# Optimization experiments

Hardware: AMD Instinct MI355X
Metric: run time of the kernel (lower is better)

The kernel has to match this reference:

```python
import jax, jax.numpy as jnp
import numpy as np

# ---- configuration matching init_kwargs ----
CTX_C = 96        # context_v_features
M_FREQS = 8       # m_encode_num_freqs
OUT_C = 45        # out_features
NDIM = 3
SIGMA = 5.0       # sigma_encode_scale
EPS = 1e-7        # TARGET_COORD_EPSILON
CX = CY = CZ = 32
QX = QY = QZ = 48
B = 1
CTX_VOX = 2.0
Q_VOX = 1.25
N_COORD = 4 * NDIM + NDIM * 2 * M_FREQS   # 60
INTERNAL = CTX_C + N_COORD                # 156


def _lin_init(k, fi, fo):
    s = 1.0 / np.sqrt(fi)
    kw, kb = jax.random.split(k)
    return (jax.random.uniform(kw, (fi, fo), jnp.float32, -s, s),
            jax.random.uniform(kb, (fo,), jnp.float32, -s, s))


def setup_inputs() -> dict:
    key = jax.random.key(0)
    ks = jax.random.split(key, 12)
    context_v = jax.random.normal(ks[0], (B, CTX_C, CX, CY, CZ), jnp.float32)
    ax = jnp.arange(CX, dtype=jnp.float32) * CTX_VOX
    gx, gy, gz = jnp.meshgrid(ax, ax, ax, indexing='ij')
    context_spatial_extent = jnp.broadcast_to(
        jnp.stack([gx, gy, gz], 0)[None], (B, 3, CX, CY, CZ)).astype(jnp.float32)
    # queries in the interior so nearest-idx + 1 stays in bounds
    query_coord = jax.random.uniform(ks[1], (B, 3, QX, QY, QZ), jnp.float32,
                                     CTX_VOX, (CX - 2) * CTX_VOX)
    query_vox_size = jnp.full((B, 3), Q_VOX, jnp.float32)
    inp = dict(context_v=context_v, context_spatial_extent=context_spatial_extent,
               query_vox_size=query_vox_size, query_coord=query_coord)
    ki = 2
    for b in range(2):
        inp[f'blk{b}_w0'], inp[f'blk{b}_b0'] = _lin_init(ks[ki], INTERNAL, CTX_C); ki += 1
        inp[f'blk{b}_w1'], inp[f'blk{b}_b1'] = _lin_init(ks[ki], CTX_C, CTX_C); ki += 1
        inp[f'blk{b}_w2'], inp[f'blk{b}_b2'] = _lin_init(ks[ki], CTX_C, CTX_C); ki += 1
    inp['post_w'], inp['post_b'] = _lin_init(ks[ki], CTX_C, OUT_C)
    return inp


def _flat(t):
    # 'b c x y z -> (b x y z) c'
    return jnp.moveaxis(t, 1, -1).reshape(-1, t.shape[1])


def _unflat(t, b, x, y, z):
    # '(b x y z) c -> b c x y z'
    return jnp.moveaxis(t.reshape(b, x, y, z, -1), -1, 1)


def _fourier(c):
    # c: (N, 3) normalized coords; geometric frequency ladder scaled by sigma
    freqs = SIGMA ** (jnp.arange(M_FREQS, dtype=c.dtype) / M_FREQS)   # (m,)
    ang = (2.0 * jnp.pi) * c[:, :, None] * freqs                      # (N,3,m)
    return jnp.concatenate([jnp.sin(ang), jnp.cos(ang)], axis=-1).reshape(c.shape[0], -1)


def _skip_block(x, coord, w0, b0, w1, b1, w2, b2):
    # SkipMLPBlock: concat(context, coord) -> 3 dense SiLU layers -> residual add
    h = jnp.concatenate([x, coord], axis=-1)
    h = jax.nn.silu(h @ w0 + b0)
    h = jax.nn.silu(h @ w1 + b1)
    h = jax.nn.silu(h @ w2 + b2)
    return x + h, coord


def _sub_grid_forward(ctx_val, ctx_coord, q_coord, ctx_vox, q_vox, p):
    # ctx_val: (B,C,X,Y,Z); coords: (B,3,X,Y,Z); ctx_vox/q_vox: (B,3,1,1,1)
    b, _, x, y, z = q_coord.shape
    rel = jnp.maximum(ctx_coord - q_coord, -ctx_vox / 2 + EPS)
    rel_norm = (rel - jnp.min(rel, axis=(2, 3, 4), keepdims=True)) / (1.5 * ctx_vox)
    enc = _fourier(_flat(rel_norm))                                   # (N, 6m)
    qv = jnp.broadcast_to(q_vox, rel_norm.shape)
    coord_feats = jnp.concatenate(
        [_flat(qv), _flat(ctx_coord), _flat(q_coord), _flat(rel_norm), enc], axis=-1)
    h = _flat(ctx_val)
    xc = coord_feats
    for i in range(2):
        h, xc = _skip_block(h, xc, p[f'blk{i}_w0'], p[f'blk{i}_b0'],
                            p[f'blk{i}_w1'], p[f'blk{i}_b1'],
                            p[f'blk{i}_w2'], p[f'blk{i}_b2'])
    pred = h @ p['post_w'] + p['post_b']
    return _unflat(pred, b, x, y, z), rel


def reference(context_v, context_spatial_extent, query_vox_size, query_coord,
              blk0_w0, blk0_b0, blk0_w1, blk0_b1, blk0_w2, blk0_b2,
              blk1_w0, blk1_b0, blk1_w1, blk1_b1, blk1_w2, blk1_b2,
              post_w, post_b):
    p = dict(blk0_w0=blk0_w0, blk0_b0=blk0_b0, blk0_w1=blk0_w1, blk0_b1=blk0_b1,
             blk0_w2=blk0_w2, blk0_b2=blk0_b2, blk1_w0=blk1_w0, blk1_b0=blk1_b0,
             blk1_w1=blk1_w1, blk1_b1=blk1_b1, blk1_w2=blk1_w2, blk1_b2=blk1_b2,
             post_w=post_w, post_b=post_b)
    bsz, _, qx, qy, qz = query_coord.shape
    cx, cy, cz = context_spatial_extent.shape[2:]
    ctx_vox = jnp.abs(context_spatial_extent[..., 1, 1, 1]
                      - context_spatial_extent[..., 0, 0, 0])[:, :, None, None, None]
    q_vox = query_vox_size[:, :, None, None, None]
    # nearest context voxel index per query point (regular grid)
    origin = context_spatial_extent[:, :, 0, 0, 0][:, :, None, None, None]
    nearest = jnp.round((query_coord - origin) / ctx_vox).astype(jnp.int32)
    xi = jnp.clip(nearest[:, 0], 0, cx - 2).reshape(-1)
    yi = jnp.clip(nearest[:, 1], 0, cy - 2).reshape(-1)
    zi = jnp.clip(nearest[:, 2], 0, cz - 2).reshape(-1)
    b_idx = jnp.broadcast_to(jnp.arange(bsz)[:, None, None, None],
                             (bsz, qx, qy, qz)).reshape(-1)
    preds = []
    rel000 = None
    for i in (0, 1):
        for j in (0, 1):
            for k in (0, 1):
                cval = context_v[b_idx, :, xi + i, yi + j, zi + k]            # (N,C) gather
                cval = _unflat(cval, bsz, qx, qy, qz)
                ccoord = context_spatial_extent[b_idx, :, xi + i, yi + j, zi + k]
                ccoord = _unflat(ccoord, bsz, qx, qy, qz)
                pred, rel = _sub_grid_forward(cval, ccoord, query_coord,
                                              ctx_vox, q_vox, p)
                preds.append(pred)
                if i == 0 and j == 0 and k == 0:
                    rel000 = rel
    preds = jnp.stack(preds, 0)   # (8, B, OUT, X, Y, Z)
    # trilinear combine over the 2x2x2 sub-window (grid_sample align_corners=True;
    # grid coord channel 0 indexes z_sub (W), 1 -> y_sub (H), 2 -> x_sub (D))
    g = jnp.clip((rel000 - 0.5) * 2.0, -1.0 + EPS, 1.0 - EPS)
    t = (g + 1.0) / 2.0
    tz, ty, tx = t[:, 0], t[:, 1], t[:, 2]
    out = jnp.zeros_like(preds[0])
    for i in (0, 1):
        wi = tx if i == 1 else 1.0 - tx
        for j in (0, 1):
            wj = ty if j == 1 else 1.0 - ty
            for k in (0, 1):
                wk = tz if k == 1 else 1.0 - tz
                out = out + preds[i * 4 + j * 2 + k] * (wi * wj * wk)[:, None]
    return out
```

## Files before the change

### kernel.cpp

```cpp
#include <hip/hip_runtime.h>
#include <hip/hip_bf16.h>

typedef unsigned short ushort_t;
typedef short short8 __attribute__((ext_vector_type(8)));
typedef short shrt4 __attribute__((ext_vector_type(4)));
typedef unsigned short ush4 __attribute__((ext_vector_type(4)));
typedef unsigned int uintx2 __attribute__((ext_vector_type(2)));
typedef float floatx4 __attribute__((ext_vector_type(4)));

#define SA 168
#define SW 104
#define NQ 110592
#define CVOL 32768

#define L0A   0
#define L0B   15360
#define A1_00 30720
#define A1_01 39936
#define A1_10 49152
#define A1_11 58368
#define PST   67584
#define WTOT  72192
#define BTOT  9216

#define WSW_OFF  64
#define BIAS_OFF 147456
#define CVT_OFF  196608

#if defined(__HIP_DEVICE_COMPILE__)
#define MFMA16(A, B, C) __builtin_amdgcn_mfma_f32_16x16x16bf16_1k(A, B, C, 0, 0, 0)
#else
#define MFMA16(A, B, C) (C)
#endif

#if defined(__HIP_DEVICE_COMPILE__) && __has_builtin(__builtin_amdgcn_sinf) && __has_builtin(__builtin_amdgcn_cosf) && __has_builtin(__builtin_amdgcn_fractf)
#define FAST_SINCOS 1
#else
#define FAST_SINCOS 0
#endif

__device__ __forceinline__ float bf2f(ushort_t u) { return __uint_as_float(((unsigned)u) << 16); }
__device__ __forceinline__ ushort_t f2bf(float f) {
    unsigned u = __float_as_uint(f);
    unsigned r = (u + 0x7fffu + ((u >> 16) & 1u)) >> 16;
    return (ushort_t)r;
}
__device__ __forceinline__ shrt4 pk4(floatx4 v) {
    uintx2 u;
    u[0] = (unsigned)f2bf(v[0]) | ((unsigned)f2bf(v[1]) << 16);
    u[1] = (unsigned)f2bf(v[2]) | ((unsigned)f2bf(v[3]) << 16);
    return __builtin_bit_cast(shrt4, u);
}
__device__ __forceinline__ unsigned encodeMin(float x) {
    unsigned u = __float_as_uint(x);
    return (u & 0x80000000u) ? ~u : (u | 0x80000000u);
}
__device__ __forceinline__ float decodeMin(unsigned key) {
    unsigned u = (key & 0x80000000u) ? (key ^ 0x80000000u) : ~key;
    return __uint_as_float(u);
}

__device__ __constant__ float FREQ[8] = {
    1.0f, 1.2228445f, 1.4953488f, 1.8285791f,
    2.2360680f, 2.7343640f, 3.3437015f, 4.0888269f
};

__global__ void decoder_txp(const float* __restrict__ cv, ushort_t* __restrict__ cvT) {
    __shared__ ushort_t ld[128 * SW];
    int tid = threadIdx.x;
    int base = blockIdx.x * 128;
    int cl = tid & 127, h = tid >> 7;
    #pragma unroll 4
    for (int ch = h * 48; ch < h * 48 + 48; ++ch)
        ld[cl * SW + ch] = f2bf(cv[ch * CVOL + base + cl]);
    __syncthreads();
    #pragma unroll
    for (int it = 0; it < 6; ++it) {
        int idx = it * 256 + tid;
        int r = idx / 12, c = idx - r * 12;
        *(uint4*)&cvT[(base + r) * 96 + c * 8] = *(const uint4*)&ld[r * SW + c * 8];
    }
}

__global__ void decoder_prep(const float* __restrict__ w00, const float* __restrict__ b00,
                             const float* __restrict__ w01, const float* __restrict__ b01,
                             const float* __restrict__ w02, const float* __restrict__ b02,
                             const float* __restrict__ w10, const float* __restrict__ b10,
                             const float* __restrict__ w11, const float* __restrict__ b11,
                             const float* __restrict__ w12, const float* __restrict__ b12,
                             const float* __restrict__ pw, ushort_t* __restrict__ wsW,
                             float* __restrict__ biasF, unsigned* __restrict__ keys) {
    int idx = blockIdx.x * 256 + threadIdx.x;
    if (idx < 3) keys[idx] = 0xFFFFFFFFu;
    if (idx >= WTOT + BTOT) return;
    if (idx >= WTOT) {
        int t = idx - WTOT;
        int layer = t / 1536, rem = t - layer * 1536;
        int mt = rem >> 8, l2i = rem & 255;
        int lane = l2i >> 2, r = l2i & 3;
        int m = mt * 16 + (lane >> 4) * 4 + r;
        const float* B = layer == 0 ? b00 : layer == 1 ? b01 : layer == 2 ? b02
                       : layer == 3 ? b10 : layer == 4 ? b11 : b12;
        biasF[t] = B[m];
        return;
    }
    ushort_t v = 0;
    if (idx < A1_00) {
        const float* W = (idx < L0B) ? w00 : w10;
        int li = idx - ((idx < L0B) ? L0A : L0B);
        int j = li & 7, lane = (li >> 3) & 63, chunk = li >> 9;
        int kc = chunk % 5, mt = chunk / 5;
        int k = kc * 32 + (lane >> 4) * 8 + j;
        int m = mt * 16 + (lane & 15);
        if (k < 156) v = f2bf(W[k * 96 + m]);
    } else if (idx < PST) {
        const float* W = idx < A1_01 ? w01 : idx < A1_10 ? w02 : idx < A1_11 ? w11 : w12;
        int off = idx < A1_01 ? A1_00 : idx < A1_10 ? A1_01 : idx < A1_11 ? A1_10 : A1_11;
        int li = idx - off;
        int i = li & 3, kl = (li >> 2) & 1, lane = (li >> 3) & 63, chunk = li >> 9;
        int kp = chunk % 3, mt = chunk / 3;
        int k = (kp * 2 + kl) * 16 + (lane >> 4) * 4 + i;
        int m = mt * 16 + (lane & 15);
        v = f2bf(W[k * 96 + m]);
    } else {
        int li = idx - PST;
        int j = li & 7, lane = (li >> 3) & 63, chunk = li >> 9;
        int kc = chunk % 3, t = chunk / 3;
        int k = kc * 32 + (lane >> 4) * 8 + j;
        int n = t * 16 + (lane & 15);
        if (n < 45) v = f2bf(pw[k * 45 + n]);
    }
    wsW[idx] = v;
}

__global__ void decoder_prepass(const float* __restrict__ qc, const float* __restrict__ ext,
                                unsigned* __restrict__ keys) {
    __shared__ unsigned mk[3];
    int tid = threadIdx.x;
    int lane = tid & 63;
    if (tid < 3) mk[tid] = 0xFFFFFFFFu;
    __syncthreads();
    int p = blockIdx.x * 256 + tid;
    #pragma unroll
    for (int c = 0; c < 3; ++c) {
        float org = ext[c * CVOL];
        float vox = fabsf(ext[c * CVOL + 1057] - org);
        float q = qc[c * NQ + p];
        float nf = rintf((q - org) / vox);
        int ci = (int)nf; ci = ci < 0 ? 0 : (ci > 30 ? 30 : ci);
        float base = org + (float)ci * vox - q;
        for (int off = 32; off > 0; off >>= 1) base = fminf(base, __shfl_xor(base, off));
        if (lane == 0) atomicMin(&mk[c], encodeMin(base));
    }
    __syncthreads();
    if (tid < 3) atomicMin(&keys[tid], mk[tid]);
}

__global__ __launch_bounds__(256, 3) void decoder_main(
    const ushort_t* __restrict__ cvT, const float* __restrict__ ext,
    const float* __restrict__ qvx, const float* __restrict__ qc,
    const float* __restrict__ pb, const ushort_t* __restrict__ wsW,
    const float* __restrict__ biasF,
    const unsigned* __restrict__ minKeys, float* __restrict__ out)
{
    __shared__ ushort_t Xin[128 * SA];
    __shared__ ushort_t Hhat[16 * SW];
    __shared__ float ptQ[3][16], ptBase[3][16], ptT[3][16];
    __shared__ int ptCI[3][16];
    __shared__ float wcorn[16][8];

    const int tid = threadIdx.x;
    const int lane = tid & 63;
    const int wv = tid >> 6;
    const int quad = lane >> 4;
    const int l16 = lane & 15;
    const int lane8 = lane << 3, quad8 = quad * 8, quad4 = quad * 4;
    const int p0 = blockIdx.x * 16;
    const int col0 = wv * 32;

    float vox[3], org[3], lim[3], inv3v[3], qv[3], mrel[3][2];
    #pragma unroll
    for (int c = 0; c < 3; ++c) {
        org[c] = ext[c * CVOL];
        vox[c] = fabsf(ext[c * CVOL + 1057] - org[c]);
        lim[c] = -0.5f * vox[c] + 1e-7f;
        inv3v[c] = 1.0f / (1.5f * vox[c]);
        qv[c] = qvx[c];
        float mb = decodeMin(minKeys[c]);
        mrel[c][0] = fmaxf(mb, lim[c]);
        mrel[c][1] = fmaxf(mb + vox[c], lim[c]);
    }

    if (tid < 64) {
        int p = tid >> 2, c = tid & 3;
        if (c < 3) {
            float q = qc[c * NQ + p0 + p];
            float nf = rintf((q - org[c]) / vox[c]);
            int ci = (int)nf; ci = ci < 0 ? 0 : (ci > 30 ? 30 : ci);
            float base = org[c] + (float)ci * vox[c] - q;
            float rel0 = fmaxf(base, lim[c]);
            float g = fminf(fmaxf((rel0 - 0.5f) * 2.0f, -1.0f + 1e-7f), 1.0f - 1e-7f);
            ptQ[c][p] = q; ptCI[c][p] = ci; ptBase[c][p] = base; ptT[c][p] = (g + 1.0f) * 0.5f;
        }
    }
    __syncthreads();

    if (tid < 128) {
        int p = tid >> 3, corner = tid & 7;
        int i = corner >> 2, j = (corner >> 1) & 1, k = corner & 1;
        float wx = i ? ptT[2][p] : 1.0f - ptT[2][p];
        float wy = j ? ptT[1][p] : 1.0f - ptT[1][p];
        float wz = k ? ptT[0][p] : 1.0f - ptT[0][p];
        wcorn[p][corner] = wx * wy * wz;
    }

    {
        const int r = tid >> 1, h = tid & 1;
        const int p = r >> 3, corner = r & 7;
        const int i0 = corner >> 2, i1 = (corner >> 1) & 1, i2 = corner & 1;
        int io[3] = {i0, i1, i2};

        int cell = (ptCI[0][p] + i0) * 1024 + (ptCI[1][p] + i1) * 32 + ptCI[2][p] + i2;
        const uint4* src = (const uint4*)&cvT[cell * 96];
        uint4* dstX = (uint4*)&Xin[r * SA];
        #pragma unroll
        for (int cc = h * 6; cc < h * 6 + 6; ++cc) dstX[cc] = src[cc];

        float rn[3];
        #pragma unroll
        for (int c = 0; c < 3; ++c) {
            float rel = fmaxf(ptBase[c][p] + (float)io[c] * vox[c], lim[c]);
            rn[c] = (rel - mrel[c][io[c]]) * inv3v[c];
        }
        ushort_t* row = &Xin[r * SA];
        if (h == 0) {
            #pragma unroll
            for (int c = 0; c < 3; ++c) {
                row[96 + c]  = f2bf(qv[c]);
                row[99 + c]  = f2bf(org[c] + (float)(ptCI[c][p] + io[c]) * vox[c]);
                row[102 + c] = f2bf(ptQ[c][p]);
                row[105 + c] = f2bf(rn[c]);
            }
            #pragma unroll
            for (int z = 156; z < SA; ++z) row[z] = 0;
            #pragma unroll
            for (int m = 0; m < 8; ++m) {
                float ang = rn[0] * FREQ[m];
#if FAST_SINCOS
                float fr = __builtin_amdgcn_fractf(ang);
                row[108 + m] = f2bf(__builtin_amdgcn_sinf(fr));
                row[116 + m] = f2bf(__builtin_amdgcn_cosf(fr));
#else
                float s, co; sincospif(2.0f * ang, &s, &co);
                row[108 + m] = f2bf(s); row[116 + m] = f2bf(co);
#endif
            }
        } else {
            #pragma unroll
            for (int c = 1; c < 3; ++c) {
                #pragma unroll
                for (int m = 0; m < 8; ++m) {
                    float ang = rn[c] * FREQ[m];
#if FAST_SINCOS
                    float fr = __builtin_amdgcn_fractf(ang);
                    row[108 + c * 16 + m] = f2bf(__builtin_amdgcn_sinf(fr));
                    row[108 + c * 16 + 8 + m] = f2bf(__builtin_amdgcn_cosf(fr));
#else
                    float s, co; sincospif(2.0f * ang, &s, &co);
                    row[108 + c * 16 + m] = f2bf(s);
                    row[108 + c * 16 + 8 + m] = f2bf(co);
#endif
                }
            }
        }
    }
    __syncthreads();

    const int A32off[2] = {L0A, L0B};
    const int A16off[2][2] = {{A1_00, A1_01}, {A1_10, A1_11}};
    floatx4 acc[6][2];
    shrt4 bfr[6][2];

    #pragma unroll
    for (int blk = 0; blk < 2; ++blk) {
        {
            short8 bX[2][5];
            #pragma unroll
            for (int nt = 0; nt < 2; ++nt)
                #pragma unroll
                for (int kc = 0; kc < 5; ++kc)
                    bX[nt][kc] = *(const short8*)&Xin[(col0 + nt * 16 + l16) * SA + kc * 32 + quad8];
            #pragma unroll
            for (int mt = 0; mt < 6; ++mt) {
                short8 aw[5];
                #pragma unroll
                for (int kc = 0; kc < 5; ++kc)
                    aw[kc] = *(const short8*)&wsW[A32off[blk] + ((mt * 5 + kc) << 9) + lane8];
                #pragma unroll
                for (int nt = 0; nt < 2; ++nt) {
                    floatx4 a = {0.f, 0.f, 0.f, 0.f};
                    #pragma unroll
                    for (int kc = 0; kc < 5; ++kc)
                        a = __builtin_amdgcn_mfma_f32_16x16x32_bf16(aw[kc], bX[nt][kc], a, 0, 0, 0);
                    acc[mt][nt] = a;
                }
            }
        }
        {
            const int lay = blk * 3;
            #pragma unroll
            for (int mt = 0; mt < 6; ++mt) {
                floatx4 bv = *(const floatx4*)&biasF[((lay * 6 + mt) << 8) + (lane << 2)];
                #pragma unroll
                for (int nt = 0; nt < 2; ++nt) {
                    floatx4 s;
                    #pragma unroll
                    for (int r = 0; r < 4; ++r) {
                        float z = acc[mt][nt][r] + bv[r];
                        s[r] = z * __builtin_amdgcn_rcpf(1.0f + __expf(-z));
                    }
                    bfr[mt][nt] = pk4(s);
                }
            }
        }
        #pragma unroll
        for (int l = 1; l < 3; ++l) {
            #pragma unroll
            for (int mt = 0; mt < 6; ++mt) {
                short8 awp[3];
                #pragma unroll
                for (int kp = 0; kp < 3; ++kp)
                    awp[kp] = *(const short8*)&wsW[A16off[blk][l - 1] + ((mt * 3 + kp) << 9) + lane8];
                #pragma unroll
                for (int nt = 0; nt < 2; ++nt) {
                    floatx4 a = {0.f, 0.f, 0.f, 0.f};
                    #pragma unroll
                    for (int kc = 0; kc < 6; ++kc) {
                        shrt4 af = (kc & 1)
                            ? __builtin_shufflevector(awp[kc >> 1], awp[kc >> 1], 4, 5, 6, 7)
                            : __builtin_shufflevector(awp[kc >> 1], awp[kc >> 1], 0, 1, 2, 3);
                        a = MFMA16(af, bfr[kc][nt], a);
                    }
                    acc[mt][nt] = a;
                }
            }
            const int lay = blk * 3 + l;
            if (l == 1) {
                #pragma unroll
                for (int mt = 0; mt < 6; ++mt) {
                    floatx4 bv = *(const floatx4*)&biasF[((lay * 6 + mt) << 8) + (lane << 2)];
                    #pragma unroll
                    for (int nt = 0; nt < 2; ++nt) {
                        floatx4 s;
                        #pragma unroll
                        for (int r = 0; r < 4; ++r) {
                            float z = acc[mt][nt][r] + bv[r];
                            s[r] = z * __builtin_amdgcn_rcpf(1.0f + __expf(-z));
                        }
                        bfr[mt][nt] = pk4(s);
                    }
                }
            } else {
                #pragma unroll
                for (int mt = 0; mt < 6; ++mt) {
                    floatx4 bv = *(const floatx4*)&biasF[((lay * 6 + mt) << 8) + (lane << 2)];
                    #pragma unroll
                    for (int nt = 0; nt < 2; ++nt) {
                        int ca = (col0 + nt * 16 + l16) * SA + mt * 16 + quad4;
                        ush4 hu = *(const ush4*)&Xin[ca];
                        floatx4 s;
                        #pragma unroll
                        for (int r = 0; r < 4; ++r) {
                            float z = acc[mt][nt][r] + bv[r];
                            s[r] = z * __builtin_amdgcn_rcpf(1.0f + __expf(-z)) + bf2f(hu[r]);
                        }
                        uintx2 w;
                        w[0] = (unsigned)f2bf(s[0]) | ((unsigned)f2bf(s[1]) << 16);
                        w[1] = (unsigned)f2bf(s[2]) | ((unsigned)f2bf(s[3]) << 16);
                        *(uintx2*)&Xin[ca] = w;
                    }
                }
            }
        }
    }

    {
        int p = tid >> 4, s6 = (tid & 15) * 6;
        float w8[8];
        #pragma unroll
        for (int c = 0; c < 8; ++c) w8[c] = wcorn[p][c];
        #pragma unroll
        for (int cc = 0; cc < 6; ++cc) {
            int col = s6 + cc;
            float sum = 0.f;
            #pragma unroll
            for (int c = 0; c < 8; ++c) sum += w8[c] * bf2f(Xin[(p * 8 + c) * SA + col]);
            Hhat[p * SW + col] = f2bf(sum);
        }
    }
    __syncthreads();

    if (wv < 3) {
        const ushort_t* wb = wsW + PST;
        floatx4 pacc = {0.f, 0.f, 0.f, 0.f};
        #pragma unroll
        for (int kc = 0; kc < 3; ++kc) {
            short8 a = *(const short8*)&Hhat[l16 * SW + kc * 32 + quad8];
            short8 bfrag = *(const short8*)&wb[((wv * 3 + kc) << 9) + lane8];
            pacc = __builtin_amdgcn_mfma_f32_16x16x32_bf16(a, bfrag, pacc, 0, 0, 0);
        }
        int n = 16 * wv + l16;
        if (n < 45) {
            float bv = pb[n];
            float4 v;
            v.x = pacc[0] + bv; v.y = pacc[1] + bv; v.z = pacc[2] + bv; v.w = pacc[3] + bv;
            *(float4*)&out[n * NQ + p0 + quad * 4] = v;
        }
    }
}

extern "C" void kernel_launch(void* const* d_in, const int* in_sizes, int n_in,
                              void* d_out, int out_size, void* d_ws, size_t ws_size,
                              hipStream_t stream) {
    (void)in_sizes; (void)n_in; (void)out_size; (void)ws_size;
    const float* cv  = (const float*)d_in[0];
    const float* ext = (const float*)d_in[1];
    const float* qvx = (const float*)d_in[2];
    const float* qc  = (const float*)d_in[3];
    const float* w00 = (const float*)d_in[4];
    const float* b00 = (const float*)d_in[5];
    const float* w01 = (const float*)d_in[6];
    const float* b01 = (const float*)d_in[7];
    const float* w02 = (const float*)d_in[8];
    const float* b02 = (const float*)d_in[9];
    const float* w10 = (const float*)d_in[10];
    const float* b10 = (const float*)d_in[11];
    const float* w11 = (const float*)d_in[12];
    const float* b11 = (const float*)d_in[13];
    const float* w12 = (const float*)d_in[14];
    const float* b12 = (const float*)d_in[15];
    const float* pw  = (const float*)d_in[16];
    const float* pb  = (const float*)d_in[17];

    unsigned* keys = (unsigned*)d_ws;
    ushort_t* wsW  = (ushort_t*)((char*)d_ws + WSW_OFF);
    float* biasF   = (float*)((char*)d_ws + BIAS_OFF);
    ushort_t* cvT  = (ushort_t*)((char*)d_ws + CVT_OFF);

    decoder_txp<<<256, 256, 0, stream>>>(cv, cvT);
    decoder_prep<<<318, 256, 0, stream>>>(w00, b00, w01, b01, w02, b02,
                                          w10, b10, w11, b11, w12, b12,
                                          pw, wsW, biasF, keys);
    decoder_prepass<<<432, 256, 0, stream>>>(qc, ext, keys);
    decoder_main<<<6912, 256, 0, stream>>>(cvT, ext, qvx, qc,
                                           pb, wsW, biasF, keys, (float*)d_out);
}
```

Before: 356.7 us.

## Merge prep kernels, fold bias into MFMA init, use packed bf16 conversions

Merges the three pre-processing kernels (transpose, weight prep, min-key prepass) into one launch that dispatches on block index, and initializes the keys with a memset instead. In the main kernel the bias is loaded as the MFMA accumulator's initial value instead of being added afterwards, float-to-bf16 packing uses a hardware packed-convert builtin when available, and the corner-weighted reduction reads bf16 pairs as 32-bit words. Together these aim to cut launch overhead and ALU work in the epilogues. The fallback pack rounds differently from round-to-nearest-even, and the memset adds a separate stream operation.

New measurement: 322.9 us. 1.1x faster.

```diff
diff --git a/kernel.cpp b/kernel.cpp
--- a/kernel.cpp
+++ b/kernel.cpp
@@ -27,6 +27,10 @@
 #define BIAS_OFF 147456
 #define CVT_OFF  196608
 
+#define TXP_NB   256
+#define PREP_NB  318
+#define PRE_NB   (TXP_NB + PREP_NB + 432)
+
 #if defined(__HIP_DEVICE_COMPILE__)
 #define MFMA16(A, B, C) __builtin_amdgcn_mfma_f32_16x16x16bf16_1k(A, B, C, 0, 0, 0)
 #else
@@ -45,10 +49,19 @@
     unsigned r = (u + 0x7fffu + ((u >> 16) & 1u)) >> 16;
     return (ushort_t)r;
 }
+__device__ __forceinline__ unsigned pkpair(float a, float b) {
+#if defined(__HIP_DEVICE_COMPILE__) && __has_builtin(__builtin_amdgcn_cvt_pk_bf16_f32)
+    return __builtin_bit_cast(unsigned, __builtin_amdgcn_cvt_pk_bf16_f32(a, b));
+#else
+    unsigned ua = __float_as_uint(a) + 0x8000u;
+    unsigned ub = __float_as_uint(b) + 0x8000u;
+    return __builtin_amdgcn_perm(ub, ua, 0x07060302);
+#endif
+}
 __device__ __forceinline__ shrt4 pk4(floatx4 v) {
     uintx2 u;
-    u[0] = (unsigned)f2bf(v[0]) | ((unsigned)f2bf(v[1]) << 16);
-    u[1] = (unsigned)f2bf(v[2]) | ((unsigned)f2bf(v[3]) << 16);
+    u[0] = pkpair(v[0], v[1]);
+    u[1] = pkpair(v[2], v[3]);
     return __builtin_bit_cast(shrt4, u);
 }
 __device__ __forceinline__ unsigned encodeMin(float x) {
@@ -65,95 +78,99 @@
     2.2360680f, 2.7343640f, 3.3437015f, 4.0888269f
 };
 
-__global__ void decoder_txp(const float* __restrict__ cv, ushort_t* __restrict__ cvT) {
+__global__ void decoder_pre(const float* __restrict__ cv, ushort_t* __restrict__ cvT,
+                            const float* __restrict__ w00, const float* __restrict__ b00,
+                            const float* __restrict__ w01, const float* __restrict__ b01,
+                            const float* __restrict__ w02, const float* __restrict__ b02,
+                            const float* __restrict__ w10, const float* __restrict__ b10,
+                            const float* __restrict__ w11, const float* __restrict__ b11,
+                            const float* __restrict__ w12, const float* __restrict__ b12,
+                            const float* __restrict__ pw, ushort_t* __restrict__ wsW,
+                            float* __restrict__ biasF,
+                            const float* __restrict__ qc, const float* __restrict__ ext,
+                            unsigned* __restrict__ keys) {
     __shared__ ushort_t ld[128 * SW];
-    int tid = threadIdx.x;
-    int base = blockIdx.x * 128;
-    int cl = tid & 127, h = tid >> 7;
-    #pragma unroll 4
-    for (int ch = h * 48; ch < h * 48 + 48; ++ch)
-        ld[cl * SW + ch] = f2bf(cv[ch * CVOL + base + cl]);
-    __syncthreads();
-    #pragma unroll
-    for (int it = 0; it < 6; ++it) {
-        int idx = it * 256 + tid;
-        int r = idx / 12, c = idx - r * 12;
-        *(uint4*)&cvT[(base + r) * 96 + c * 8] = *(const uint4*)&ld[r * SW + c * 8];
-    }
-}
-
-__global__ void decoder_prep(const float* __restrict__ w00, const float* __restrict__ b00,
-                             const float* __restrict__ w01, const float* __restrict__ b01,
-                             const float* __restrict__ w02, const float* __restrict__ b02,
-                             const float* __restrict__ w10, const float* __restrict__ b10,
-                             const float* __restrict__ w11, const float* __restrict__ b11,
-                             const float* __restrict__ w12, const float* __restrict__ b12,
-                             const float* __restrict__ pw, ushort_t* __restrict__ wsW,
-                             float* __restrict__ biasF, unsigned* __restrict__ keys) {
-    int idx = blockIdx.x * 256 + threadIdx.x;
-    if (idx < 3) keys[idx] = 0xFFFFFFFFu;
-    if (idx >= WTOT + BTOT) return;
-    if (idx >= WTOT) {
-        int t = idx - WTOT;
-        int layer = t / 1536, rem = t - layer * 1536;
-        int mt = rem >> 8, l2i = rem & 255;
-        int lane = l2i >> 2, r = l2i & 3;
-        int m = mt * 16 + (lane >> 4) * 4 + r;
-        const float* B = layer == 0 ? b00 : layer == 1 ? b01 : layer == 2 ? b02
-                       : layer == 3 ? b10 : layer == 4 ? b11 : b12;
-        biasF[t] = B[m];
+    __shared__ unsigned mk[3];
+    const int bx = blockIdx.x;
+    const int tid = threadIdx.x;
+
+    if (bx < TXP_NB) {
+        int base = bx * 128;
+        int cl = tid & 127, h = tid >> 7;
+        #pragma unroll 4
+        for (int ch = h * 48; ch < h * 48 + 48; ++ch)
+            ld[cl * SW + ch] = f2bf(cv[ch * CVOL + base + cl]);
+        __syncthreads();
+        #pragma unroll
+        for (int it = 0; it < 6; ++it) {
+            int idx = it * 256 + tid;
+            int r = idx / 12, c = idx - r * 12;
+            *(uint4*)&cvT[(base + r) * 96 + c * 8] = *(const uint4*)&ld[r * SW + c * 8];
+        }
         return;
     }
-    ushort_t v = 0;
-    if (idx < A1_00) {
-        const float* W = (idx < L0B) ? w00 : w10;
-        int li = idx - ((idx < L0B) ? L0A : L0B);
-        int j = li & 7, lane = (li >> 3) & 63, chunk = li >> 9;
-        int kc = chunk % 5, mt = chunk / 5;
-        int k = kc * 32 + (lane >> 4) * 8 + j;
-        int m = mt * 16 + (lane & 15);
-        if (k < 156) v = f2bf(W[k * 96 + m]);
-    } else if (idx < PST) {
-        const float* W = idx < A1_01 ? w01 : idx < A1_10 ? w02 : idx < A1_11 ? w11 : w12;
-        int off = idx < A1_01 ? A1_00 : idx < A1_10 ? A1_01 : idx < A1_11 ? A1_10 : A1_11;
-        int li = idx - off;
-        int i = li & 3, kl = (li >> 2) & 1, lane = (li >> 3) & 63, chunk = li >> 9;
-        int kp = chunk % 3, mt = chunk / 3;
-        int k = (kp * 2 + kl) * 16 + (lane >> 4) * 4 + i;
-        int m = mt * 16 + (lane & 15);
-        v = f2bf(W[k * 96 + m]);
-    } else {
-        int li = idx - PST;
-        int j = li & 7, lane = (li >> 3) & 63, chunk = li >> 9;
-        int kc = chunk % 3, t = chunk / 3;
-        int k = kc * 32 + (lane >> 4) * 8 + j;
-        int n = t * 16 + (lane & 15);
-        if (n < 45) v = f2bf(pw[k * 45 + n]);
-    }
-    wsW[idx] = v;
-}
-
-__global__ void decoder_prepass(const float* __restrict__ qc, const float* __restrict__ ext,
-                                unsigned* __restrict__ keys) {
-    __shared__ unsigned mk[3];
-    int tid = threadIdx.x;
-    int lane = tid & 63;
-    if (tid < 3) mk[tid] = 0xFFFFFFFFu;
-    __syncthreads();
-    int p = blockIdx.x * 256 + tid;
-    #pragma unroll
-    for (int c = 0; c < 3; ++c) {
-        float org = ext[c * CVOL];
-        float vox = fabsf(ext[c * CVOL + 1057] - org);
-        float q = qc[c * NQ + p];
-        float nf = rintf((q - org) / vox);
-        int ci = (int)nf; ci = ci < 0 ? 0 : (ci > 30 ? 30 : ci);
-        float base = org + (float)ci * vox - q;
-        for (int off = 32; off > 0; off >>= 1) base = fminf(base, __shfl_xor(base, off));
-        if (lane == 0) atomicMin(&mk[c], encodeMin(base));
-    }
-    __syncthreads();
-    if (tid < 3) atomicMin(&keys[tid], mk[tid]);
+    if (bx < TXP_NB + PREP_NB) {
+        int idx = (bx - TXP_NB) * 256 + tid;
+        if (idx >= WTOT + BTOT) return;
+        if (idx >= WTOT) {
+            int t = idx - WTOT;
+            int layer = t / 1536, rem = t - layer * 1536;
+            int mt = rem >> 8, l2i = rem & 255;
+            int lane = l2i >> 2, r = l2i & 3;
+            int m = mt * 16 + (lane >> 4) * 4 + r;
+            const float* B = layer == 0 ? b00 : layer == 1 ? b01 : layer == 2 ? b02
+                           : layer == 3 ? b10 : layer == 4 ? b11 : b12;
+            biasF[t] = B[m];
+            return;
+        }
+        ushort_t v = 0;
+        if (idx < A1_00) {
+            const float* W = (idx < L0B) ? w00 : w10;
+            int li = idx - ((idx < L0B) ? L0A : L0B);
+            int j = li & 7, lane = (li >> 3) & 63, chunk = li >> 9;
+            int kc = chunk % 5, mt = chunk / 5;
+            int k = kc * 32 + (lane >> 4) * 8 + j;
+            int m = mt * 16 + (lane & 15);
+            if (k < 156) v = f2bf(W[k * 96 + m]);
+        } else if (idx < PST) {
+            const float* W = idx < A1_01 ? w01 : idx < A1_10 ? w02 : idx < A1_11 ? w11 : w12;
+            int off = idx < A1_01 ? A1_00 : idx < A1_10 ? A1_01 : idx < A1_11 ? A1_10 : A1_11;
+            int li = idx - off;
+            int i = li & 3, kl = (li >> 2) & 1, lane = (li >> 3) & 63, chunk = li >> 9;
+            int kp = chunk % 3, mt = chunk / 3;
+            int k = (kp * 2 + kl) * 16 + (lane >> 4) * 4 + i;
+            int m = mt * 16 + (lane & 15);
+            v = f2bf(W[k * 96 + m]);
+        } else {
+            int li = idx - PST;
+            int j = li & 7, lane = (li >> 3) & 63, chunk = li >> 9;
+            int kc = chunk % 3, t = chunk / 3;
+            int k = kc * 32 + (lane >> 4) * 8 + j;
+            int n = t * 16 + (lane & 15);
+            if (n < 45) v = f2bf(pw[k * 45 + n]);
+        }
+        wsW[idx] = v;
+        return;
+    }
+    {
+        int lane = tid & 63;
+        if (tid < 3) mk[tid] = 0xFFFFFFFFu;
+        __syncthreads();
+        int p = (bx - TXP_NB - PREP_NB) * 256 + tid;
+        #pragma unroll
+        for (int c = 0; c < 3; ++c) {
+            float org = ext[c * CVOL];
+            float vox = fabsf(ext[c * CVOL + 1057] - org);
+            float q = qc[c * NQ + p];
+            float nf = rintf((q - org) / vox);
+            int ci = (int)nf; ci = ci < 0 ? 0 : (ci > 30 ? 30 : ci);
+            float base = org + (float)ci * vox - q;
+            for (int off = 32; off > 0; off >>= 1) base = fminf(base, __shfl_xor(base, off));
+            if (lane == 0) atomicMin(&mk[c], encodeMin(base));
+        }
+        __syncthreads();
+        if (tid < 3) atomicMin(&keys[tid], mk[tid]);
+    }
 }
 
 __global__ __launch_bounds__(256, 3) void decoder_main(
@@ -290,52 +307,54 @@
                 #pragma unroll
                 for (int kc = 0; kc < 5; ++kc)
                     bX[nt][kc] = *(const short8*)&Xin[(col0 + nt * 16 + l16) * SA + kc * 32 + quad8];
+            const int lay = blk * 3;
             #pragma unroll
             for (int mt = 0; mt < 6; ++mt) {
                 short8 aw[5];
                 #pragma unroll
                 for (int kc = 0; kc < 5; ++kc)
                     aw[kc] = *(const short8*)&wsW[A32off[blk] + ((mt * 5 + kc) << 9) + lane8];
+                floatx4 bv = *(const floatx4*)&biasF[((lay * 6 + mt) << 8) + (lane << 2)];
                 #pragma unroll
                 for (int nt = 0; nt < 2; ++nt) {
-                    floatx4 a = {0.f, 0.f, 0.f, 0.f};
+                    floatx4 a = __builtin_amdgcn_mfma_f32_16x16x32_bf16(aw[0], bX[nt][0], bv, 0, 0, 0);
                     #pragma unroll
-                    for (int kc = 0; kc < 5; ++kc)
+                    for (int kc = 1; kc < 5; ++kc)
                         a = __builtin_amdgcn_mfma_f32_16x16x32_bf16(aw[kc], bX[nt][kc], a, 0, 0, 0);
                     acc[mt][nt] = a;
                 }
             }
         }
         {
-            const int lay = blk * 3;
-            #pragma unroll
-            for (int mt = 0; mt < 6; ++mt) {
-                floatx4 bv = *(const floatx4*)&biasF[((lay * 6 + mt) << 8) + (lane << 2)];
+            #pragma unroll
+            for (int mt = 0; mt < 6; ++mt)
                 #pragma unroll
                 for (int nt = 0; nt < 2; ++nt) {
                     floatx4 s;
                     #pragma unroll
                     for (int r = 0; r < 4; ++r) {
-                        float z = acc[mt][nt][r] + bv[r];
+                        float z = acc[mt][nt][r];
                         s[r] = z * __builtin_amdgcn_rcpf(1.0f + __expf(-z));
                     }
                     bfr[mt][nt] = pk4(s);
                 }
-            }
         }
         #pragma unroll
         for (int l = 1; l < 3; ++l) {
+            const int lay = blk * 3 + l;
             #pragma unroll
             for (int mt = 0; mt < 6; ++mt) {
                 short8 awp[3];
                 #pragma unroll
                 for (int kp = 0; kp < 3; ++kp)
                     awp[kp] = *(const short8*)&wsW[A16off[blk][l - 1] + ((mt * 3 + kp) << 9) + lane8];
+                floatx4 bv = *(const floatx4*)&biasF[((lay * 6 + mt) << 8) + (lane << 2)];
                 #pragma unroll
                 for (int nt = 0; nt < 2; ++nt) {
-                    floatx4 a = {0.f, 0.f, 0.f, 0.f};
+                    shrt4 a0 = __builtin_shufflevector(awp[0], awp[0], 0, 1, 2, 3);
+                    floatx4 a = MFMA16(a0, bfr[0][nt], bv);
                     #pragma unroll
-                    for (int kc = 0; kc < 6; ++kc) {
+                    for (int kc = 1; kc < 6; ++kc) {
                         shrt4 af = (kc & 1)
                             ? __builtin_shufflevector(awp[kc >> 1], awp[kc >> 1], 4, 5, 6, 7)
                             : __builtin_shufflevector(awp[kc >> 1], awp[kc >> 1], 0, 1, 2, 3);
@@ -344,26 +363,22 @@
                     acc[mt][nt] = a;
                 }
             }
-            const int lay = blk * 3 + l;
             if (l == 1) {
                 #pragma unroll
-                for (int mt = 0; mt < 6; ++mt) {
-                    floatx4 bv = *(const floatx4*)&biasF[((lay * 6 + mt) << 8) + (lane << 2)];
+                for (int mt = 0; mt < 6; ++mt)
                     #pragma unroll
                     for (int nt = 0; nt < 2; ++nt) {
                         floatx4 s;
                         #pragma unroll
                         for (int r = 0; r < 4; ++r) {
-                            float z = acc[mt][nt][r] + bv[r];
+                            float z = acc[mt][nt][r];
                             s[r] = z * __builtin_amdgcn_rcpf(1.0f + __expf(-z));
                         }
                         bfr[mt][nt] = pk4(s);
                     }
-                }
             } else {
                 #pragma unroll
-                for (int mt = 0; mt < 6; ++mt) {
-                    floatx4 bv = *(const floatx4*)&biasF[((lay * 6 + mt) << 8) + (lane << 2)];
+                for (int mt = 0; mt < 6; ++mt)
                     #pragma unroll
                     for (int nt = 0; nt < 2; ++nt) {
                         int ca = (col0 + nt * 16 + l16) * SA + mt * 16 + quad4;
@@ -371,15 +386,14 @@
                         floatx4 s;
                         #pragma unroll
                         for (int r = 0; r < 4; ++r) {
-                            float z = acc[mt][nt][r] + bv[r];
+                            float z = acc[mt][nt][r];
                             s[r] = z * __builtin_amdgcn_rcpf(1.0f + __expf(-z)) + bf2f(hu[r]);
                         }
                         uintx2 w;
-                        w[0] = (unsigned)f2bf(s[0]) | ((unsigned)f2bf(s[1]) << 16);
-                        w[1] = (unsigned)f2bf(s[2]) | ((unsigned)f2bf(s[3]) << 16);
+                        w[0] = pkpair(s[0], s[1]);
+                        w[1] = pkpair(s[2], s[3]);
                         *(uintx2*)&Xin[ca] = w;
                     }
-                }
             }
         }
     }
@@ -389,14 +403,21 @@
         float w8[8];
         #pragma unroll
         for (int c = 0; c < 8; ++c) w8[c] = wcorn[p][c];
-        #pragma unroll
-        for (int cc = 0; cc < 6; ++cc) {
-            int col = s6 + cc;
-            float sum = 0.f;
-            #pragma unroll
-            for (int c = 0; c < 8; ++c) sum += w8[c] * bf2f(Xin[(p * 8 + c) * SA + col]);
-            Hhat[p * SW + col] = f2bf(sum);
-        }
+        float sum[6] = {0.f, 0.f, 0.f, 0.f, 0.f, 0.f};
+        #pragma unroll
+        for (int c = 0; c < 8; ++c) {
+            const unsigned* rp = (const unsigned*)&Xin[(p * 8 + c) * SA + s6];
+            float w = w8[c];
+            #pragma unroll
+            for (int d = 0; d < 3; ++d) {
+                unsigned u = rp[d];
+                sum[d * 2]     += w * __uint_as_float(u << 16);
+                sum[d * 2 + 1] += w * __uint_as_float(u & 0xFFFF0000u);
+            }
+        }
+        unsigned* hp = (unsigned*)&Hhat[p * SW + s6];
+        #pragma unroll
+        for (int d = 0; d < 3; ++d) hp[d] = pkpair(sum[d * 2], sum[d * 2 + 1]);
     }
     __syncthreads();
 
@@ -447,11 +468,11 @@
     float* biasF   = (float*)((char*)d_ws + BIAS_OFF);
     ushort_t* cvT  = (ushort_t*)((char*)d_ws + CVT_OFF);
 
-    decoder_txp<<<256, 256, 0, stream>>>(cv, cvT);
-    decoder_prep<<<318, 256, 0, stream>>>(w00, b00, w01, b01, w02, b02,
-                                          w10, b10, w11, b11, w12, b12,
-                                          pw, wsW, biasF, keys);
-    decoder_prepass<<<432, 256, 0, stream>>>(qc, ext, keys);
+    hipMemsetAsync(keys, 0xFF, 12, stream);
+    decoder_pre<<<PRE_NB, 256, 0, stream>>>(cv, cvT,
+                                            w00, b00, w01, b01, w02, b02,
+                                            w10, b10, w11, b11, w12, b12,
+                                            pw, wsW, biasF, qc, ext, keys);
     decoder_main<<<6912, 256, 0, stream>>>(cvT, ext, qvx, qc,
                                            pb, wsW, biasF, keys, (float*)d_out);
 }
```
